# Performance work log

Measured on AMD Instinct MI355X. Metric: run time of the kernel, lower is better.

The kernel has to match this reference:

```python
import jax, jax.numpy as jnp
import numpy as np

B, S, H = 1, 2048, 4096
NH, NKV, HD = 32, 8, 128
N_REP = NH // NKV
SCALING = HD ** -0.5
ROPE_THETA = 10000.0
NEG_INF = -1e9


def setup_inputs() -> dict:
    key = jax.random.key(0)
    ks = jax.random.split(key, 5)
    hidden_states = jax.random.normal(ks[0], (B, S, H), dtype=jnp.float32)
    # torch nn.Linear weights are [out_features, in_features]
    wq = jax.random.normal(ks[1], (NH * HD, H), dtype=jnp.float32) * 0.02
    wk = jax.random.normal(ks[2], (NKV * HD, H), dtype=jnp.float32) * 0.02
    wv = jax.random.normal(ks[3], (NKV * HD, H), dtype=jnp.float32) * 0.02
    wo = jax.random.normal(ks[4], (NH * HD, H), dtype=jnp.float32).T * 0.02  # [H, NH*HD] -> store as [out,in]=[H,4096]
    wo = jnp.asarray(wo)
    # RoPE tables: [1, S, HD]
    inv_freq = 1.0 / (ROPE_THETA ** (jnp.arange(0, HD, 2, dtype=jnp.float32) / HD))
    pos = jnp.arange(S, dtype=jnp.float32)
    freqs = pos[:, None] * inv_freq[None, :]            # [S, HD/2]
    emb = jnp.concatenate([freqs, freqs], axis=-1)      # [S, HD]
    cos = jnp.cos(emb)[None]
    sin = jnp.sin(emb)[None]
    # additive causal mask [1, 1, S, S]
    causal = jnp.tril(jnp.ones((S, S), dtype=bool))
    attn_mask = jnp.where(causal, 0.0, NEG_INF).astype(jnp.float32)[None, None]
    return {"hidden_states": hidden_states, "wq": wq, "wk": wk, "wv": wv,
            "wo": wo, "cos": cos, "sin": sin, "attn_mask": attn_mask}


def rotate_half(x):
    x1, x2 = jnp.split(x, 2, axis=-1)
    return jnp.concatenate([-x2, x1], axis=-1)


def reference(hidden_states, wq, wk, wv, wo, cos, sin, attn_mask):
    b, s, _ = hidden_states.shape
    # projections (x @ W.T), reshape to [B, heads, S, HD]
    q = (hidden_states @ wq.T).reshape(b, s, NH, HD).transpose(0, 2, 1, 3)
    k = (hidden_states @ wk.T).reshape(b, s, NKV, HD).transpose(0, 2, 1, 3)
    v = (hidden_states @ wv.T).reshape(b, s, NKV, HD).transpose(0, 2, 1, 3)
    # RoPE (unsqueeze_dim=1)
    c = cos[:, None]  # [1,1,S,HD]
    sn = sin[:, None]
    q = q * c + rotate_half(q) * sn
    k = k * c + rotate_half(k) * sn
    # GQA head repeat
    k = jnp.repeat(k, N_REP, axis=1)  # [B, NH, S, HD]
    v = jnp.repeat(v, N_REP, axis=1)
    # eager attention
    scores = jnp.einsum('bhqd,bhkd->bhqk', q, k) * SCALING + attn_mask[:, :, :, :s]
    attn_weights = jax.nn.softmax(scores.astype(jnp.float32), axis=-1).astype(q.dtype)
    attn_out = jnp.einsum('bhqk,bhkd->bhqd', attn_weights, v)
    attn_out = attn_out.transpose(0, 2, 1, 3).reshape(b, s, NH * HD)
    out = attn_out @ wo.T
    return out, attn_weights
```

## Files before the change

### kernel.cpp

```cpp
#include <hip/hip_runtime.h>
#include <cstdint>
#include <cstddef>


#define SEQ 2048
#define HID 4096
#define NH_ 32
#define NKV_ 8
#define HD_ 128
#define KDIM_KV 1024
#define SCALING 0.08838834764831843f

typedef __bf16 bf16;
typedef __attribute__((ext_vector_type(8))) __bf16 bf16x8;
typedef __attribute__((ext_vector_type(4))) float f32x4;

__device__ __forceinline__ unsigned short f2bf(float f) {
  __bf16 h = (__bf16)f;
  return __builtin_bit_cast(unsigned short, h);
}
__device__ __forceinline__ float bf2f(unsigned short u) {
  unsigned int x = ((unsigned int)u) << 16;
  return __builtin_bit_cast(float, x);
}

__device__ __forceinline__ void async16(const void* g, void* l) {
  __builtin_amdgcn_global_load_lds(
      (const __attribute__((address_space(1))) unsigned int*)g,
      (__attribute__((address_space(3))) unsigned int*)l, 16, 0, 0);
}

__device__ __forceinline__ void cvt_one(const float* __restrict__ src,
                                        bf16* __restrict__ dst, int i) {
  float4 v = ((const float4*)src)[i];
  union { unsigned short u[4]; uint2 vv; } pk;
  pk.u[0] = f2bf(v.x); pk.u[1] = f2bf(v.y);
  pk.u[2] = f2bf(v.z); pk.u[3] = f2bf(v.w);
  ((uint2*)dst)[i] = pk.vv;
}

__global__ __launch_bounds__(256) void cvt_kernel(const float* __restrict__ src,
                                                  bf16* __restrict__ dst, int n4) {
  int i = blockIdx.x * 256 + threadIdx.x;
  if (i >= n4) return;
  cvt_one(src, dst, i);
}

__global__ __launch_bounds__(256) void cvt4_kernel(
    const float* __restrict__ hs, const float* __restrict__ wq,
    const float* __restrict__ wk, const float* __restrict__ wv,
    bf16* __restrict__ hsb, bf16* __restrict__ wqb,
    bf16* __restrict__ wkb, bf16* __restrict__ wvb) {
  int i = blockIdx.x * 256 + threadIdx.x;
  if (i < 2097152) { cvt_one(hs, hsb, i); return; }
  i -= 2097152;
  if (i < 4194304) { cvt_one(wq, wqb, i); return; }
  i -= 4194304;
  if (i < 1048576) { cvt_one(wk, wkb, i); return; }
  i -= 1048576;
  cvt_one(wv, wvb, i);
}

template <int AR>
__device__ __forceinline__ void gemm256_loop(const char* __restrict__ Ab,
                                             const char* __restrict__ Bb,
                                             char* smem,
                                             f32x4 (&acc)[AR * 4][4]) {
  const int NT = 128;
  const int tid = threadIdx.x;
  const int wid = tid >> 6, lane = tid & 63;
  const int quad = lane >> 4, l16 = lane & 15;
  const int wm = wid >> 2, wn = wid & 3;
  const int ASZ = AR * 8192;
  const int SLOT = ASZ + 16384;

  const char* gA0 = Ab + (size_t)(tid >> 2) * 8192 + (size_t)(tid & 3) * 16;
  const char* gA1 = gA0 + (size_t)128 * 8192;
  const char* gB0 = Bb + (size_t)(tid >> 2) * 8192 + (size_t)(tid & 3) * 16;
  const char* gB1 = gB0 + (size_t)128 * 8192;
  const int ldsA0 = wid * 1024;
  const int ldsB0 = ASZ + wid * 1024;

  const f32x4 fz = {0.f, 0.f, 0.f, 0.f};
#pragma unroll
  for (int m = 0; m < AR * 4; m++)
#pragma unroll
    for (int n = 0; n < 4; n++) acc[m][n] = fz;

#pragma unroll
  for (int t = 0; t < 2; t++) {
    char* sl = smem + t * SLOT;
    async16(gA0 + t * 64, sl + ldsA0);
    if (AR == 2) async16(gA1 + t * 64, sl + ldsA0 + 8192);
    async16(gB0 + t * 64, sl + ldsB0);
    async16(gB1 + t * 64, sl + ldsB0 + 8192);
  }

#pragma unroll 3
  for (int t = 0; t < NT; t++) {
    if (t + 1 < NT) {
      if (AR == 2) asm volatile("s_waitcnt vmcnt(4)" ::: "memory");
      else         asm volatile("s_waitcnt vmcnt(3)" ::: "memory");
    } else {
      asm volatile("s_waitcnt vmcnt(0)" ::: "memory");
    }
    __builtin_amdgcn_s_barrier();
    __builtin_amdgcn_sched_barrier(0);
    if (t + 2 < NT) {
      char* sl = smem + ((t + 2) % 3) * SLOT;
      async16(gA0 + (size_t)(t + 2) * 64, sl + ldsA0);
      if (AR == 2) async16(gA1 + (size_t)(t + 2) * 64, sl + ldsA0 + 8192);
    }
    const bf16* sA = (const bf16*)(smem + (t % 3) * SLOT);
    const bf16* sB = (const bf16*)(smem + (t % 3) * SLOT + ASZ);
    bf16x8 a[AR * 2], b[4];
#pragma unroll
    for (int m = 0; m < AR * 2; m++)
      a[m] = *(const bf16x8*)(sA + (size_t)(wm * (AR * 64) + m * 16 + l16) * 32 + quad * 8);
#pragma unroll
    for (int n = 0; n < 4; n++)
      b[n] = *(const bf16x8*)(sB + (size_t)(wn * 64 + n * 16 + l16) * 32 + quad * 8);
    __builtin_amdgcn_s_setprio(1);
#pragma unroll
    for (int m = 0; m < AR * 2; m++)
#pragma unroll
      for (int n = 0; n < 4; n++)
        acc[m][n] = __builtin_amdgcn_mfma_f32_16x16x32_bf16(a[m], b[n], acc[m][n], 0, 0, 0);
    __builtin_amdgcn_s_setprio(0);
    __builtin_amdgcn_s_barrier();
    __builtin_amdgcn_sched_barrier(0);
    if (t + 2 < NT) {
      char* sl = smem + ((t + 2) % 3) * SLOT;
      async16(gB0 + (size_t)(t + 2) * 64, sl + ldsB0);
      async16(gB1 + (size_t)(t + 2) * 64, sl + ldsB0 + 8192);
    }
#pragma unroll
    for (int m = 0; m < AR * 2; m++)
      a[m] = *(const bf16x8*)(sA + (size_t)(wm * (AR * 64) + (AR * 2 + m) * 16 + l16) * 32 + quad * 8);
    __builtin_amdgcn_s_setprio(1);
#pragma unroll
    for (int m = 0; m < AR * 2; m++)
#pragma unroll
      for (int n = 0; n < 4; n++)
        acc[AR * 2 + m][n] =
            __builtin_amdgcn_mfma_f32_16x16x32_bf16(a[m], b[n], acc[AR * 2 + m][n], 0, 0, 0);
    __builtin_amdgcn_s_setprio(0);
  }
}

__global__ __launch_bounds__(512, 2) void qkv_gemm(
    const bf16* __restrict__ A,
    const bf16* __restrict__ Wq,
    const bf16* __restrict__ Wk,
    const bf16* __restrict__ Wv,
    const float* __restrict__ cosp,
    const float* __restrict__ sinp,
    bf16* __restrict__ qout,
    bf16* __restrict__ kout,
    bf16* __restrict__ vtout)
{
  extern __shared__ char smem[];
  const int mi = blockIdx.x, nt = blockIdx.y;
  const int tid = threadIdx.x;
  const int wid = tid >> 6, lane = tid & 63;
  const int quad = lane >> 4, l16 = lane & 15;
  const int wm = wid >> 2, wn = wid & 3;

  const bf16* Bp;
  if (nt < 16)      Bp = Wq + (size_t)nt * 256 * HID;
  else if (nt < 20) Bp = Wk + (size_t)(nt - 16) * 256 * HID;
  else              Bp = Wv + (size_t)(nt - 20) * 256 * HID;

  f32x4 acc[8][4];
  gemm256_loop<2>((const char*)(A + (size_t)mi * 256 * HID), (const char*)Bp,
                  smem, acc);

  __syncthreads();
  float* ct = (float*)smem;
  for (int ch = 0; ch < 4; ch++) {
    if (wm == (ch >> 1)) {
#pragma unroll
      for (int mm = 0; mm < 4; mm++)
#pragma unroll
        for (int n = 0; n < 4; n++)
#pragma unroll
          for (int r = 0; r < 4; r++)
            ct[(size_t)(mm * 16 + quad * 4 + r) * 265 + wn * 64 + n * 16 + l16] =
                acc[(ch & 1) * 4 + mm][n][r];
    }
    __syncthreads();
    if (nt < 20) {
      const int r0 = tid >> 5, c8 = (tid & 31) << 3;
      bf16* outp; int ldo, colbase;
      if (nt < 16) { outp = qout; ldo = HID; colbase = nt * 256; }
      else         { outp = kout; ldo = KDIM_KV; colbase = (nt - 16) * 256; }
      const int d0 = c8 & 127;
      const bool lo = d0 < 64;
#pragma unroll
      for (int p = 0; p < 4; p++) {
        int row = p * 16 + r0;
        int s = mi * 256 + ch * 64 + row;
        union { unsigned short u[8]; uint4 v; } pk;
#pragma unroll
        for (int u8 = 0; u8 < 8; u8++) {
          int c = c8 + u8;
          float x  = ct[(size_t)row * 265 + c];
          float xp = ct[(size_t)row * 265 + (c ^ 64)];
          float cv = cosp[(size_t)s * HD_ + d0 + u8];
          float sv = sinp[(size_t)s * HD_ + d0 + u8];
          pk.u[u8] = f2bf(lo ? x * cv - xp * sv : x * cv + xp * sv);
        }
        *(uint4*)(outp + (size_t)s * ldo + colbase + c8) = pk.v;
      }
    } else {
      const int dcol = tid & 255, sb = (tid >> 8) << 3;
      const int vh = (nt - 20) * 2 + (dcol >> 7), dd = dcol & 127;
#pragma unroll
      for (int i = 0; i < 4; i++) {
        int s8 = sb + i * 16;
        union { unsigned short u[8]; uint4 v; } pk;
#pragma unroll
        for (int u8 = 0; u8 < 8; u8++)
          pk.u[u8] = f2bf(ct[(size_t)(s8 + u8) * 265 + dcol]);
        *(uint4*)(vtout + ((size_t)vh * HD_ + dd) * SEQ + mi * 256 + ch * 64 + s8) = pk.v;
      }
    }
    __syncthreads();
  }
}

__device__ __forceinline__ void stage128(const bf16* __restrict__ base, int row_stride,
                                         unsigned short (*buf)[136], int tid) {
  const int r0 = tid >> 4;
  const int c = (tid & 15) * 8;
#pragma unroll
  for (int g = 0; g < 8; g++) {
    int row = g * 16 + r0;
    uint4 v = *(const uint4*)(base + (size_t)row * row_stride + c);
    *(uint4*)&buf[row][c] = v;
  }
}

__global__ __launch_bounds__(256, 3) void attn_kernel(
    const bf16* __restrict__ qb,
    const bf16* __restrict__ kb,
    const bf16* __restrict__ vtb,
    float* __restrict__ wout,
    bf16* __restrict__ aout)
{
  const int bid = blockIdx.x;
  const int h = bid & 31;
  const int qt = 31 - (bid >> 5);
  const int kvh = h >> 2;
  const int tid = threadIdx.x;
  const int wave = tid >> 6, lane = tid & 63;
  const int quad = lane >> 4, l16 = lane & 15;
  const int kmax = qt >> 1;

  __shared__ __align__(16) unsigned short kvbuf[128][136];
  __shared__ __align__(16) unsigned short wlds[64][136];

  {
    const int kc0 = (kmax + 1) * 128;
    if (kc0 < SEQ) {
      const float4 z = make_float4(0.f, 0.f, 0.f, 0.f);
      for (int row = 0; row < 64; row++) {
        float* zrow = wout + ((size_t)h * SEQ + (size_t)qt * 64 + row) * SEQ;
        for (int c = kc0 + (tid << 2); c < SEQ; c += 1024)
          *(float4*)(zrow + c) = z;
      }
    }
  }

  bf16x8 aq[4];
  {
    const bf16* qbase = qb + ((size_t)(qt * 64) + wave * 16 + l16) * HID + h * HD_;
#pragma unroll
    for (int ks = 0; ks < 4; ks++)
      aq[ks] = *(const bf16x8*)(qbase + ks * 32 + quad * 8);
  }

  float m_[4], l_[4];
#pragma unroll
  for (int r = 0; r < 4; r++) { m_[r] = -3.0e38f; l_[r] = 0.f; }

  for (int kt = 0; kt <= kmax; kt++) {
    __syncthreads();
    stage128(kb + (size_t)(kt * 128) * KDIM_KV + kvh * HD_, KDIM_KV, kvbuf, tid);
    __syncthreads();

    f32x4 acc[8];
    const f32x4 fz = {0.f, 0.f, 0.f, 0.f};
#pragma unroll
    for (int j = 0; j < 8; j++) acc[j] = fz;
#pragma unroll
    for (int ks = 0; ks < 4; ks++) {
      bf16x8 bk[8];
#pragma unroll
      for (int j = 0; j < 8; j++)
        bk[j] = *(const bf16x8*)&kvbuf[j * 16 + l16][ks * 32 + quad * 8];
#pragma unroll
      for (int j = 0; j < 8; j++)
        acc[j] = __builtin_amdgcn_mfma_f32_16x16x32_bf16(aq[ks], bk[j], acc[j], 0, 0, 0);
    }

    const bool mc = (kt == kmax);
#pragma unroll
    for (int r = 0; r < 4; r++) {
      int qrow = qt * 64 + wave * 16 + quad * 4 + r;
      float sv[8], mx = -3.0e38f;
#pragma unroll
      for (int j = 0; j < 8; j++) {
        float s = acc[j][r] * SCALING;
        if (mc && (kt * 128 + j * 16 + l16) > qrow) s -= 1.0e9f;
        sv[j] = s;
        mx = fmaxf(mx, s);
      }
#pragma unroll
      for (int sh = 1; sh < 16; sh <<= 1) mx = fmaxf(mx, __shfl_xor(mx, sh));
      float mn = fmaxf(m_[r], mx);
      float sum = 0.f;
#pragma unroll
      for (int j = 0; j < 8; j++) sum += __expf(sv[j] - mn);
#pragma unroll
      for (int sh = 1; sh < 16; sh <<= 1) sum += __shfl_xor(sum, sh);
      l_[r] = l_[r] * __expf(m_[r] - mn) + sum;
      m_[r] = mn;
    }
  }

  float linv[4];
#pragma unroll
  for (int r = 0; r < 4; r++) linv[r] = 1.f / l_[r];

  f32x4 oac[8];
  {
    const f32x4 fz = {0.f, 0.f, 0.f, 0.f};
#pragma unroll
    for (int j = 0; j < 8; j++) oac[j] = fz;
  }

  for (int kt = 0; kt <= kmax; kt++) {
    __syncthreads();
    stage128(kb + (size_t)(kt * 128) * KDIM_KV + kvh * HD_, KDIM_KV, kvbuf, tid);
    __syncthreads();

    f32x4 acc[8];
    const f32x4 fz = {0.f, 0.f, 0.f, 0.f};
#pragma unroll
    for (int j = 0; j < 8; j++) acc[j] = fz;
#pragma unroll
    for (int ks = 0; ks < 4; ks++) {
      bf16x8 bk[8];
#pragma unroll
      for (int j = 0; j < 8; j++)
        bk[j] = *(const bf16x8*)&kvbuf[j * 16 + l16][ks * 32 + quad * 8];
#pragma unroll
      for (int j = 0; j < 8; j++)
        acc[j] = __builtin_amdgcn_mfma_f32_16x16x32_bf16(aq[ks], bk[j], acc[j], 0, 0, 0);
    }

    const bool mc = (kt == kmax);
#pragma unroll
    for (int r = 0; r < 4; r++) {
      int qrow = qt * 64 + wave * 16 + quad * 4 + r;
#pragma unroll
      for (int j = 0; j < 8; j++) {
        float s = acc[j][r] * SCALING;
        if (mc && (kt * 128 + j * 16 + l16) > qrow) s -= 1.0e9f;
        wlds[wave * 16 + quad * 4 + r][j * 16 + l16] = f2bf(__expf(s - m_[r]) * linv[r]);
      }
    }
    __syncthreads();

    stage128(vtb + (size_t)kvh * HD_ * SEQ + kt * 128, SEQ, kvbuf, tid);
    {
      float* wdst = wout + ((size_t)h * SEQ + (size_t)qt * 64) * SEQ + kt * 128;
      const int rr = tid >> 5, c4 = (tid & 31) << 2;
#pragma unroll
      for (int p = 0; p < 8; p++) {
        int row = p * 8 + rr;
        uint2 w = *(const uint2*)&wlds[row][c4];
        float4 v;
        v.x = bf2f((unsigned short)(w.x & 0xffff));
        v.y = bf2f((unsigned short)(w.x >> 16));
        v.z = bf2f((unsigned short)(w.y & 0xffff));
        v.w = bf2f((unsigned short)(w.y >> 16));
        *(float4*)(wdst + (size_t)row * SEQ + c4) = v;
      }
    }
    __syncthreads();

#pragma unroll
    for (int ks = 0; ks < 4; ks++) {
      bf16x8 aw, bv[8];
      aw = *(const bf16x8*)&wlds[wave * 16 + l16][ks * 32 + quad * 8];
#pragma unroll
      for (int j = 0; j < 8; j++)
        bv[j] = *(const bf16x8*)&kvbuf[j * 16 + l16][ks * 32 + quad * 8];
#pragma unroll
      for (int j = 0; j < 8; j++)
        oac[j] = __builtin_amdgcn_mfma_f32_16x16x32_bf16(aw, bv[j], oac[j], 0, 0, 0);
    }
  }

  __syncthreads();
#pragma unroll
  for (int j = 0; j < 8; j++)
#pragma unroll
    for (int r = 0; r < 4; r++)
      wlds[wave * 16 + quad * 4 + r][j * 16 + l16] = f2bf(oac[j][r]);
  __syncthreads();
  {
    const int r0 = tid >> 4, c8 = (tid & 15) << 3;
    bf16* abase = aout + (size_t)(qt * 64) * HID + h * HD_;
#pragma unroll
    for (int p = 0; p < 4; p++) {
      int row = p * 16 + r0;
      union { unsigned short u[8]; uint4 v; } pk;
#pragma unroll
      for (int u8 = 0; u8 < 8; u8++) pk.u[u8] = wlds[row][c8 + u8];
      *(uint4*)(abase + (size_t)row * HID + c8) = pk.v;
    }
  }
}

__global__ __launch_bounds__(512, 2) void proj_gemm(const bf16* __restrict__ A,
                                                    const bf16* __restrict__ B,
                                                    float* __restrict__ C) {
  extern __shared__ char smem[];
  const int mi = blockIdx.x, nt = blockIdx.y;
  const int tid = threadIdx.x;
  const int lane = tid & 63;
  const int wid = tid >> 6;
  const int quad = lane >> 4, l16 = lane & 15;
  const int wm = wid >> 2, wn = wid & 3;

  f32x4 acc[4][4];
  gemm256_loop<1>((const char*)(A + (size_t)mi * 128 * HID),
                  (const char*)(B + (size_t)nt * 256 * HID), smem, acc);

#pragma unroll
  for (int m = 0; m < 4; m++)
#pragma unroll
    for (int n = 0; n < 4; n++)
#pragma unroll
      for (int r = 0; r < 4; r++) {
        int row = mi * 128 + wm * 64 + m * 16 + quad * 4 + r;
        int col = nt * 256 + wn * 64 + n * 16 + l16;
        C[(size_t)row * HID + col] = acc[m][n][r];
      }
}

extern "C" void kernel_launch(void* const* d_in, const int* in_sizes, int n_in,
                              void* d_out, int out_size, void* d_ws, size_t ws_size,
                              hipStream_t stream) {
  const float* hs   = (const float*)d_in[0];
  const float* wq   = (const float*)d_in[1];
  const float* wk   = (const float*)d_in[2];
  const float* wv   = (const float*)d_in[3];
  const float* wo   = (const float*)d_in[4];
  const float* cosp = (const float*)d_in[5];
  const float* sinp = (const float*)d_in[6];

  if (ws_size < (size_t)109051904) return;

  char* ws = (char*)d_ws;
  bf16* hsb = (bf16*)(ws + 0);
  bf16* wqb = (bf16*)(ws + 16777216);
  bf16* wkb = (bf16*)(ws + 50331648);
  bf16* wvb = (bf16*)(ws + 58720256);
  bf16* qb  = (bf16*)(ws + 67108864);
  bf16* kb  = (bf16*)(ws + 83886080);
  bf16* vtb = (bf16*)(ws + 88080384);
  bf16* aob = (bf16*)(ws + 92274688);

  float* outp = (float*)d_out;
  float* wout = outp + (size_t)SEQ * HID;

  hipFuncSetAttribute((const void*)qkv_gemm,
                      hipFuncAttributeMaxDynamicSharedMemorySize, 98304);
  hipFuncSetAttribute((const void*)proj_gemm,
                      hipFuncAttributeMaxDynamicSharedMemorySize, 73728);

  cvt4_kernel<<<8388608 / 256, 256, 0, stream>>>(hs, wq, wk, wv, hsb, wqb, wkb, wvb);

  qkv_gemm<<<dim3(8, 24), 512, 98304, stream>>>(hsb, wqb, wkb, wvb, cosp, sinp, qb, kb, vtb);

  cvt_kernel<<<4194304 / 256, 256, 0, stream>>>(wo, wqb, 4194304);

  attn_kernel<<<1024, 256, 0, stream>>>(qb, kb, vtb, wout, aob);

  proj_gemm<<<dim3(16, 16), 512, 73728, stream>>>(aob, wqb, outp);
}
```

Measured before the change: 1.032 ms.

## Prefetch K/V tiles into registers to overlap global loads with compute

Splits tile staging into a global-to-register load and a register-to-LDS write. The next K or V tile is issued before the current tile's MFMA and softmax work, so global latency hides behind compute. Plain __syncthreads is replaced with raw s_barrier plus explicit vmcnt and lgkmcnt waits. This costs 8 extra uint4 registers per thread at an occupancy target of 3 blocks, and relies on hand-placed waits being correct for all in-flight memory operations.

```diff
diff --git a/kernel.cpp b/kernel.cpp
--- a/kernel.cpp
+++ b/kernel.cpp
@@ -29,6 +29,10 @@
       (const __attribute__((address_space(1))) unsigned int*)g,
       (__attribute__((address_space(3))) unsigned int*)l, 16, 0, 0);
 }
+
+#define WAIT_VM0()   asm volatile("s_waitcnt vmcnt(0)" ::: "memory")
+#define WAIT_LGKM0() asm volatile("s_waitcnt lgkmcnt(0)" ::: "memory")
+#define BAR0()  do { __builtin_amdgcn_s_barrier(); __builtin_amdgcn_sched_barrier(0); } while (0)
 
 __device__ __forceinline__ void cvt_one(const float* __restrict__ src,
                                         bf16* __restrict__ dst, int i) {
@@ -229,16 +233,21 @@
   }
 }
 
-__device__ __forceinline__ void stage128(const bf16* __restrict__ base, int row_stride,
-                                         unsigned short (*buf)[136], int tid) {
+__device__ __forceinline__ void stage_load(const bf16* __restrict__ base, int row_stride,
+                                           int tid, uint4 (&v)[8]) {
   const int r0 = tid >> 4;
   const int c = (tid & 15) * 8;
 #pragma unroll
-  for (int g = 0; g < 8; g++) {
-    int row = g * 16 + r0;
-    uint4 v = *(const uint4*)(base + (size_t)row * row_stride + c);
-    *(uint4*)&buf[row][c] = v;
-  }
+  for (int g = 0; g < 8; g++)
+    v[g] = *(const uint4*)(base + (size_t)(g * 16 + r0) * row_stride + c);
+}
+__device__ __forceinline__ void stage_write(unsigned short (*buf)[136], int tid,
+                                            const uint4 (&v)[8]) {
+  const int r0 = tid >> 4;
+  const int c = (tid & 15) * 8;
+#pragma unroll
+  for (int g = 0; g < 8; g++)
+    *(uint4*)&buf[g * 16 + r0][c] = v[g];
 }
 
 __global__ __launch_bounds__(256, 3) void attn_kernel(
@@ -260,6 +269,9 @@
   __shared__ __align__(16) unsigned short kvbuf[128][136];
   __shared__ __align__(16) unsigned short wlds[64][136];
 
+  const bf16* kbase = kb + (size_t)kvh * HD_;
+  const bf16* vbase = vtb + (size_t)kvh * HD_ * SEQ;
+
   {
     const int kc0 = (kmax + 1) * 128;
     if (kc0 < SEQ) {
@@ -284,10 +296,17 @@
 #pragma unroll
   for (int r = 0; r < 4; r++) { m_[r] = -3.0e38f; l_[r] = 0.f; }
 
+  uint4 streg[8];
+
+  stage_load(kbase, KDIM_KV, tid, streg);
   for (int kt = 0; kt <= kmax; kt++) {
-    __syncthreads();
-    stage128(kb + (size_t)(kt * 128) * KDIM_KV + kvh * HD_, KDIM_KV, kvbuf, tid);
-    __syncthreads();
+    BAR0();
+    WAIT_VM0();
+    stage_write(kvbuf, tid, streg);
+    WAIT_LGKM0();
+    BAR0();
+    if (kt < kmax)
+      stage_load(kbase + (size_t)((kt + 1) * 128) * KDIM_KV, KDIM_KV, tid, streg);
 
     f32x4 acc[8];
     const f32x4 fz = {0.f, 0.f, 0.f, 0.f};
@@ -340,10 +359,14 @@
     for (int j = 0; j < 8; j++) oac[j] = fz;
   }
 
+  stage_load(kbase, KDIM_KV, tid, streg);
   for (int kt = 0; kt <= kmax; kt++) {
-    __syncthreads();
-    stage128(kb + (size_t)(kt * 128) * KDIM_KV + kvh * HD_, KDIM_KV, kvbuf, tid);
-    __syncthreads();
+    BAR0();
+    WAIT_VM0();
+    stage_write(kvbuf, tid, streg);
+    WAIT_LGKM0();
+    BAR0();
+    stage_load(vbase + (size_t)(kt * 128), SEQ, tid, streg);
 
     f32x4 acc[8];
     const f32x4 fz = {0.f, 0.f, 0.f, 0.f};
@@ -371,9 +394,11 @@
         wlds[wave * 16 + quad * 4 + r][j * 16 + l16] = f2bf(__expf(s - m_[r]) * linv[r]);
       }
     }
-    __syncthreads();
-
-    stage128(vtb + (size_t)kvh * HD_ * SEQ + kt * 128, SEQ, kvbuf, tid);
+    WAIT_LGKM0();
+    BAR0();
+
+    WAIT_VM0();
+    stage_write(kvbuf, tid, streg);
     {
       float* wdst = wout + ((size_t)h * SEQ + (size_t)qt * 64) * SEQ + kt * 128;
       const int rr = tid >> 5, c4 = (tid & 31) << 2;
@@ -389,7 +414,10 @@
         *(float4*)(wdst + (size_t)row * SEQ + c4) = v;
       }
     }
-    __syncthreads();
+    if (kt < kmax)
+      stage_load(kbase + (size_t)((kt + 1) * 128) * KDIM_KV, KDIM_KV, tid, streg);
+    WAIT_LGKM0();
+    BAR0();
 
 #pragma unroll
     for (int ks = 0; ks < 4; ks++) {
```

New measurement: 1.355 ms. +31.4%, slower.
